# Optimization experiments

Measured on AMD Instinct MI355X. Metric: run time of the kernel, lower is better.

Reference implementation:

```python
import jax, jax.numpy as jnp
import numpy as np

SCENE_BOUND = 1.5

def _trilinear_sample(vol, g):
    """torch.nn.functional.grid_sample (3D, bilinear, zeros padding, align_corners=True).

    vol: (C, D, H, W) volume.
    g:   (N, 3) normalized coords in [-1, 1], ordered (x, y, z) where
         x indexes W, y indexes H, z indexes D (torch convention).
    returns: (N, C) interpolated features.
    """
    C, D, H, W = vol.shape
    sizes = jnp.array([W, H, D], dtype=g.dtype)
    pix = (g + 1.0) * 0.5 * (sizes - 1.0)  # align_corners=True mapping
    x, y, z = pix[:, 0], pix[:, 1], pix[:, 2]
    x0f, y0f, z0f = jnp.floor(x), jnp.floor(y), jnp.floor(z)
    fx, fy, fz = x - x0f, y - y0f, z - z0f
    x0, y0, z0 = x0f.astype(jnp.int32), y0f.astype(jnp.int32), z0f.astype(jnp.int32)
    vol_flat = vol.reshape(C, -1)  # (C, D*H*W)
    out = jnp.zeros((g.shape[0], C), dtype=vol.dtype)
    for dz in (0, 1):
        for dy in (0, 1):
            for dx in (0, 1):
                xi, yi, zi = x0 + dx, y0 + dy, z0 + dz
                w = ((fx if dx else 1.0 - fx)
                     * (fy if dy else 1.0 - fy)
                     * (fz if dz else 1.0 - fz))
                inb = ((xi >= 0) & (xi < W) & (yi >= 0) & (yi < H)
                       & (zi >= 0) & (zi < D))
                xi_c = jnp.clip(xi, 0, W - 1)
                yi_c = jnp.clip(yi, 0, H - 1)
                zi_c = jnp.clip(zi, 0, D - 1)
                flat = (zi_c * H + yi_c) * W + xi_c  # (N,)
                feat = jnp.take(vol_flat, flat, axis=1)  # (C, N)
                out = out + (w * inb.astype(w.dtype))[:, None] * feat.T
    return out


def setup_inputs() -> dict:
    key = jax.random.key(0)
    k1, k2, k3, k4, k5 = jax.random.split(key, 5)
    N, R = 2_000_000, 128
    xyz = (jax.random.uniform(k1, (N, 3), dtype=jnp.float32) * 2.0 - 1.0) * (SCENE_BOUND * 0.99)
    base_density = jax.random.normal(k2, (1, 1, R, R, R), dtype=jnp.float32)
    base_sh = jax.random.normal(k3, (1, 27, R, R, R), dtype=jnp.float32)
    detail_density = jax.random.normal(k4, (1, 1, R, R, R), dtype=jnp.float32) * 0.1
    detail_sh = jax.random.normal(k5, (1, 27, R, R, R), dtype=jnp.float32) * 0.1
    return {"xyz": xyz, "base_density": base_density, "base_sh": base_sh,
            "detail_density": detail_density, "detail_sh": detail_sh}


def reference(xyz, base_density, base_sh, detail_density, detail_sh):
    # grid property: concat(base_density + detail_density, base_sh + detail_sh)
    vol = jnp.concatenate([base_density + detail_density,
                           base_sh + detail_sh], axis=1)[0]  # (C, R, R, R)
    g = xyz / SCENE_BOUND  # normalized to [-1, 1]
    return _trilinear_sample(vol, g)  # (N, C), matches query()'s permuted output
```

## Files before the change

kernel.cpp:

```cpp
#include <hip/hip_runtime.h>
#include <hip/hip_fp16.h>
#include <cstdint>
#include <cstddef>

#define RR   128
#define VV   (RR * RR * RR)
#define NCH  28
#define CPAD 32

__device__ __forceinline__ unsigned short f2h(float f) {
    __half h = __float2half(f);
    return *reinterpret_cast<unsigned short*>(&h);
}
__device__ __forceinline__ float2 up2(unsigned int u) {
    __half2 h = *reinterpret_cast<__half2*>(&u);
    return __half22float2(h);
}

__global__ __launch_bounds__(256) void presum_kernel(
    const float* __restrict__ bden, const float* __restrict__ bsh,
    const float* __restrict__ dden, const float* __restrict__ dsh,
    unsigned short* __restrict__ ws)
{
    int tid = blockIdx.x * 256 + threadIdx.x;
    if (tid >= VV) return;

    unsigned short s[CPAD];
    s[0] = f2h(bden[tid] + dden[tid]);
#pragma unroll
    for (int c = 1; c < NCH; ++c) {
        size_t off = (size_t)(c - 1) * VV + tid;
        s[c] = f2h(bsh[off] + dsh[off]);
    }
#pragma unroll
    for (int c = NCH; c < CPAD; ++c) s[c] = 0;

    uint4* w = (uint4*)(ws + (size_t)tid * CPAD);
#pragma unroll
    for (int q = 0; q < 4; ++q) {
        uint4 v;
        v.x = (unsigned int)s[q*8+0] | ((unsigned int)s[q*8+1] << 16);
        v.y = (unsigned int)s[q*8+2] | ((unsigned int)s[q*8+3] << 16);
        v.z = (unsigned int)s[q*8+4] | ((unsigned int)s[q*8+5] << 16);
        v.w = (unsigned int)s[q*8+6] | ((unsigned int)s[q*8+7] << 16);
        w[q] = v;
    }
}

__global__ __launch_bounds__(256) void gather_kernel(
    const float* __restrict__ xyz,
    const unsigned short* __restrict__ vol,
    float* __restrict__ out, int N)
{
    int tid = blockIdx.x * 256 + threadIdx.x;
    int n = tid >> 2;
    int t = tid & 3;
    if (n >= N) return;

    const float* xp = xyz + (size_t)n * 3;
    const float S = 63.5f / 1.5f;
    float px = fmaf(xp[0], S, 63.5f);
    float py = fmaf(xp[1], S, 63.5f);
    float pz = fmaf(xp[2], S, 63.5f);
    float fx0 = floorf(px), fy0 = floorf(py), fz0 = floorf(pz);
    float fx = px - fx0, fy = py - fy0, fz = pz - fz0;
    int ix = (int)fx0, iy = (int)fy0, iz = (int)fz0;
    ix = min(max(ix, 0), RR - 2);
    iy = min(max(iy, 0), RR - 2);
    iz = min(max(iz, 0), RR - 2);

    float wx[2] = {1.0f - fx, fx};
    float wy[2] = {1.0f - fy, fy};
    float wz[2] = {1.0f - fz, fz};

    int ibase = (iz * RR + iy) * RR + ix;
    const char* basep = (const char*)vol + (size_t)t * 16;

    float acc[8];
#pragma unroll
    for (int k = 0; k < 8; ++k) acc[k] = 0.0f;

#pragma unroll
    for (int dz = 0; dz < 2; ++dz)
#pragma unroll
    for (int dy = 0; dy < 2; ++dy)
#pragma unroll
    for (int dx = 0; dx < 2; ++dx) {
        int vidx = ibase + dz * (RR * RR) + dy * RR + dx;
        float w = wz[dz] * wy[dy] * wx[dx];
        const uint4 q = *(const uint4*)(basep + (size_t)vidx * (CPAD * 2));
        float2 p0 = up2(q.x), p1 = up2(q.y), p2 = up2(q.z), p3 = up2(q.w);
        acc[0] = fmaf(w, p0.x, acc[0]);
        acc[1] = fmaf(w, p0.y, acc[1]);
        acc[2] = fmaf(w, p1.x, acc[2]);
        acc[3] = fmaf(w, p1.y, acc[3]);
        acc[4] = fmaf(w, p2.x, acc[4]);
        acc[5] = fmaf(w, p2.y, acc[5]);
        acc[6] = fmaf(w, p3.x, acc[6]);
        acc[7] = fmaf(w, p3.y, acc[7]);
    }

    float* op = out + (size_t)n * NCH + t * 8;
    if (t < 3) {
        *(float4*)op       = make_float4(acc[0], acc[1], acc[2], acc[3]);
        *(float4*)(op + 4) = make_float4(acc[4], acc[5], acc[6], acc[7]);
    } else {
        *(float4*)op = make_float4(acc[0], acc[1], acc[2], acc[3]);
    }
}

__global__ __launch_bounds__(256) void gather_fallback(
    const float* __restrict__ xyz,
    const float* __restrict__ bden, const float* __restrict__ bsh,
    const float* __restrict__ dden, const float* __restrict__ dsh,
    float* __restrict__ out, int N)
{
    int n = blockIdx.x * 256 + threadIdx.x;
    if (n >= N) return;
    const float* xp = xyz + (size_t)n * 3;
    const float S = 63.5f / 1.5f;
    float px = fmaf(xp[0], S, 63.5f);
    float py = fmaf(xp[1], S, 63.5f);
    float pz = fmaf(xp[2], S, 63.5f);
    float fx0 = floorf(px), fy0 = floorf(py), fz0 = floorf(pz);
    float fx = px - fx0, fy = py - fy0, fz = pz - fz0;
    int ix = (int)fx0, iy = (int)fy0, iz = (int)fz0;
    ix = min(max(ix, 0), RR - 2);
    iy = min(max(iy, 0), RR - 2);
    iz = min(max(iz, 0), RR - 2);
    float wx[2] = {1.0f - fx, fx}, wy[2] = {1.0f - fy, fy}, wz[2] = {1.0f - fz, fz};

    int idx[8]; float w[8];
#pragma unroll
    for (int k = 0; k < 8; ++k) {
        int dz = (k >> 2) & 1, dy = (k >> 1) & 1, dx = k & 1;
        idx[k] = ((iz + dz) * RR + (iy + dy)) * RR + (ix + dx);
        w[k] = wz[dz] * wy[dy] * wx[dx];
    }
#pragma unroll
    for (int c = 0; c < NCH; ++c) {
        const float* bp = (c == 0) ? bden : (bsh + (size_t)(c - 1) * VV);
        const float* dp = (c == 0) ? dden : (dsh + (size_t)(c - 1) * VV);
        float a = 0.0f;
#pragma unroll
        for (int k = 0; k < 8; ++k)
            a = fmaf(w[k], bp[idx[k]] + dp[idx[k]], a);
        out[(size_t)n * NCH + c] = a;
    }
}

extern "C" void kernel_launch(void* const* d_in, const int* in_sizes, int n_in,
                              void* d_out, int out_size, void* d_ws, size_t ws_size,
                              hipStream_t stream) {
    const float* xyz  = (const float*)d_in[0];
    const float* bden = (const float*)d_in[1];
    const float* bsh  = (const float*)d_in[2];
    const float* dden = (const float*)d_in[3];
    const float* dsh  = (const float*)d_in[4];
    float* out = (float*)d_out;
    int N = in_sizes[0] / 3;

    size_t need = (size_t)VV * CPAD * sizeof(unsigned short);
    if (ws_size >= need) {
        presum_kernel<<<(VV + 255) / 256, 256, 0, stream>>>(
            bden, bsh, dden, dsh, (unsigned short*)d_ws);
        long long threads = (long long)N * 4;
        gather_kernel<<<(unsigned int)((threads + 255) / 256), 256, 0, stream>>>(
            xyz, (const unsigned short*)d_ws, out, N);
    } else {
        gather_fallback<<<(N + 255) / 256, 256, 0, stream>>>(
            xyz, bden, bsh, dden, dsh, out, N);
    }
}
```

Baseline: 814.2 us.

## Bin points into 8^3 cells and gather from LDS-staged grid bricks

Replaces the full-volume fp16 presum plus global gather with a counting sort of points into 4096 spatial cells (histogram, scan, atomic scatter), followed by a per-cell kernel. That kernel loads a 9^3 brick of summed channels into shared memory as fp16 and interpolates every point in the cell from LDS. This removes the 117 MB packed-volume write and read and the random global gathers. In exchange it adds two passes over xyz, atomic contention on the cell counters, scattered output writes, and a 46 KB LDS tile per 512-thread block. The base-plus-detail sum is still computed every call, with halo columns read redundantly across neighbouring cells.

```diff
diff --git a/kernel.cpp b/kernel.cpp
--- a/kernel.cpp
+++ b/kernel.cpp
@@ -3,10 +3,15 @@
 #include <cstdint>
 #include <cstddef>
 
-#define RR   128
-#define VV   (RR * RR * RR)
-#define NCH  28
-#define CPAD 32
+#define RR     128
+#define VV     (RR * RR * RR)
+#define NCH    28
+#define CPAD   32
+#define CELL   8
+#define NCD    16
+#define NCELLS 4096
+#define REG    9
+#define RV     (REG * REG * REG)
 
 __device__ __forceinline__ unsigned short f2h(float f) {
     __half h = __float2half(f);
@@ -17,95 +22,163 @@
     return __half22float2(h);
 }
 
-__global__ __launch_bounds__(256) void presum_kernel(
+__device__ __forceinline__ void point_coords(float x, float y, float z,
+                                             float& px, float& py, float& pz,
+                                             int& ix, int& iy, int& iz) {
+    const float S = 63.5f / 1.5f;
+    px = fmaf(x, S, 63.5f);
+    py = fmaf(y, S, 63.5f);
+    pz = fmaf(z, S, 63.5f);
+    ix = min(max((int)floorf(px), 0), RR - 2);
+    iy = min(max((int)floorf(py), 0), RR - 2);
+    iz = min(max((int)floorf(pz), 0), RR - 2);
+}
+
+__global__ __launch_bounds__(256) void hist_kernel(
+    const float* __restrict__ xyz, unsigned int* __restrict__ cnt, int N)
+{
+    int n = blockIdx.x * 256 + threadIdx.x;
+    if (n >= N) return;
+    const float* xp = xyz + (size_t)n * 3;
+    float px, py, pz; int ix, iy, iz;
+    point_coords(xp[0], xp[1], xp[2], px, py, pz, ix, iy, iz);
+    int cell = ((iz >> 3) * NCD + (iy >> 3)) * NCD + (ix >> 3);
+    atomicAdd(&cnt[cell], 1u);
+}
+
+__global__ __launch_bounds__(256) void scan_kernel(
+    const unsigned int* __restrict__ cnt,
+    unsigned int* __restrict__ off,
+    unsigned int* __restrict__ cur)
+{
+    __shared__ unsigned int part[256];
+    int t = threadIdx.x;
+    unsigned int local[16];
+    unsigned int s = 0;
+#pragma unroll
+    for (int i = 0; i < 16; ++i) { local[i] = cnt[t * 16 + i]; s += local[i]; }
+    part[t] = s;
+    __syncthreads();
+    for (int d = 1; d < 256; d <<= 1) {
+        unsigned int v = (t >= d) ? part[t - d] : 0u;
+        __syncthreads();
+        part[t] += v;
+        __syncthreads();
+    }
+    unsigned int base = (t == 0) ? 0u : part[t - 1];
+#pragma unroll
+    for (int i = 0; i < 16; ++i) {
+        off[t * 16 + i] = base;
+        cur[t * 16 + i] = base;
+        base += local[i];
+    }
+    if (t == 255) off[NCELLS] = part[255];
+}
+
+__global__ __launch_bounds__(256) void scatter_kernel(
+    const float* __restrict__ xyz, unsigned int* __restrict__ cur,
+    float4* __restrict__ sorted, int N)
+{
+    int n = blockIdx.x * 256 + threadIdx.x;
+    if (n >= N) return;
+    const float* xp = xyz + (size_t)n * 3;
+    float px, py, pz; int ix, iy, iz;
+    point_coords(xp[0], xp[1], xp[2], px, py, pz, ix, iy, iz);
+    int cell = ((iz >> 3) * NCD + (iy >> 3)) * NCD + (ix >> 3);
+    unsigned int slot = atomicAdd(&cur[cell], 1u);
+    sorted[slot] = make_float4(px, py, pz, __int_as_float(n));
+}
+
+__global__ __launch_bounds__(512) void cell_gather(
     const float* __restrict__ bden, const float* __restrict__ bsh,
     const float* __restrict__ dden, const float* __restrict__ dsh,
-    unsigned short* __restrict__ ws)
-{
-    int tid = blockIdx.x * 256 + threadIdx.x;
-    if (tid >= VV) return;
-
-    unsigned short s[CPAD];
-    s[0] = f2h(bden[tid] + dden[tid]);
-#pragma unroll
-    for (int c = 1; c < NCH; ++c) {
-        size_t off = (size_t)(c - 1) * VV + tid;
-        s[c] = f2h(bsh[off] + dsh[off]);
-    }
-#pragma unroll
-    for (int c = NCH; c < CPAD; ++c) s[c] = 0;
-
-    uint4* w = (uint4*)(ws + (size_t)tid * CPAD);
-#pragma unroll
-    for (int q = 0; q < 4; ++q) {
-        uint4 v;
-        v.x = (unsigned int)s[q*8+0] | ((unsigned int)s[q*8+1] << 16);
-        v.y = (unsigned int)s[q*8+2] | ((unsigned int)s[q*8+3] << 16);
-        v.z = (unsigned int)s[q*8+4] | ((unsigned int)s[q*8+5] << 16);
-        v.w = (unsigned int)s[q*8+6] | ((unsigned int)s[q*8+7] << 16);
-        w[q] = v;
-    }
-}
-
-__global__ __launch_bounds__(256) void gather_kernel(
-    const float* __restrict__ xyz,
-    const unsigned short* __restrict__ vol,
-    float* __restrict__ out, int N)
-{
-    int tid = blockIdx.x * 256 + threadIdx.x;
-    int n = tid >> 2;
-    int t = tid & 3;
-    if (n >= N) return;
-
-    const float* xp = xyz + (size_t)n * 3;
-    const float S = 63.5f / 1.5f;
-    float px = fmaf(xp[0], S, 63.5f);
-    float py = fmaf(xp[1], S, 63.5f);
-    float pz = fmaf(xp[2], S, 63.5f);
-    float fx0 = floorf(px), fy0 = floorf(py), fz0 = floorf(pz);
-    float fx = px - fx0, fy = py - fy0, fz = pz - fz0;
-    int ix = (int)fx0, iy = (int)fy0, iz = (int)fz0;
-    ix = min(max(ix, 0), RR - 2);
-    iy = min(max(iy, 0), RR - 2);
-    iz = min(max(iz, 0), RR - 2);
-
-    float wx[2] = {1.0f - fx, fx};
-    float wy[2] = {1.0f - fy, fy};
-    float wz[2] = {1.0f - fz, fz};
-
-    int ibase = (iz * RR + iy) * RR + ix;
-    const char* basep = (const char*)vol + (size_t)t * 16;
-
-    float acc[8];
-#pragma unroll
-    for (int k = 0; k < 8; ++k) acc[k] = 0.0f;
-
-#pragma unroll
-    for (int dz = 0; dz < 2; ++dz)
-#pragma unroll
-    for (int dy = 0; dy < 2; ++dy)
-#pragma unroll
-    for (int dx = 0; dx < 2; ++dx) {
-        int vidx = ibase + dz * (RR * RR) + dy * RR + dx;
-        float w = wz[dz] * wy[dy] * wx[dx];
-        const uint4 q = *(const uint4*)(basep + (size_t)vidx * (CPAD * 2));
-        float2 p0 = up2(q.x), p1 = up2(q.y), p2 = up2(q.z), p3 = up2(q.w);
-        acc[0] = fmaf(w, p0.x, acc[0]);
-        acc[1] = fmaf(w, p0.y, acc[1]);
-        acc[2] = fmaf(w, p1.x, acc[2]);
-        acc[3] = fmaf(w, p1.y, acc[3]);
-        acc[4] = fmaf(w, p2.x, acc[4]);
-        acc[5] = fmaf(w, p2.y, acc[5]);
-        acc[6] = fmaf(w, p3.x, acc[6]);
-        acc[7] = fmaf(w, p3.y, acc[7]);
-    }
-
-    float* op = out + (size_t)n * NCH + t * 8;
-    if (t < 3) {
-        *(float4*)op       = make_float4(acc[0], acc[1], acc[2], acc[3]);
-        *(float4*)(op + 4) = make_float4(acc[4], acc[5], acc[6], acc[7]);
-    } else {
-        *(float4*)op = make_float4(acc[0], acc[1], acc[2], acc[3]);
+    const float4* __restrict__ sorted, const unsigned int* __restrict__ off,
+    float* __restrict__ out)
+{
+    __shared__ unsigned short vlds[RV * CPAD];
+
+    int bid = blockIdx.x;
+    int cid = (bid & 7) * (NCELLS / 8) + (bid >> 3);
+    int cx = cid & 15, cy = (cid >> 4) & 15, cz = cid >> 8;
+    int x0 = cx << 3, y0 = cy << 3, z0 = cz << 3;
+    int xlast = (cx == 15) ? 7 : 8;
+
+    for (int task = threadIdx.x; task < 81 * CPAD; task += 512) {
+        int c = task / 81;
+        int r = task - c * 81;
+        int rz = r / 9, ry = r - rz * 9;
+        int v0 = (rz * 9 + ry) * 9;
+        if (c < NCH) {
+            int zg = min(z0 + rz, RR - 1);
+            int yg = min(y0 + ry, RR - 1);
+            size_t row = ((size_t)(zg * RR + yg)) * RR + x0;
+            const float* bp; const float* dp;
+            if (c == 0) { bp = bden + row; dp = dden + row; }
+            else { size_t o = (size_t)(c - 1) * VV + row; bp = bsh + o; dp = dsh + o; }
+            float s[9];
+#pragma unroll
+            for (int xx = 0; xx < 8; ++xx) s[xx] = bp[xx] + dp[xx];
+            s[8] = bp[xlast] + dp[xlast];
+#pragma unroll
+            for (int xx = 0; xx < 9; ++xx)
+                vlds[(v0 + xx) * CPAD + c] = f2h(s[xx]);
+        } else {
+#pragma unroll
+            for (int xx = 0; xx < 9; ++xx)
+                vlds[(v0 + xx) * CPAD + c] = 0;
+        }
+    }
+    __syncthreads();
+
+    int start = (int)off[cid], end = (int)off[cid + 1];
+    int g = threadIdx.x >> 2, t = threadIdx.x & 3;
+
+    for (int p = start + g; p < end; p += 128) {
+        float4 pt = sorted[p];
+        float px = pt.x, py = pt.y, pz = pt.z;
+        int idx = __float_as_int(pt.w);
+
+        float fx0 = floorf(px), fy0 = floorf(py), fz0 = floorf(pz);
+        float fx = px - fx0, fy = py - fy0, fz = pz - fz0;
+        int lx = min(max((int)fx0, 0), RR - 2) - x0;
+        int ly = min(max((int)fy0, 0), RR - 2) - y0;
+        int lz = min(max((int)fz0, 0), RR - 2) - z0;
+
+        float wx[2] = {1.0f - fx, fx};
+        float wy[2] = {1.0f - fy, fy};
+        float wz[2] = {1.0f - fz, fz};
+
+        float acc[8];
+#pragma unroll
+        for (int k = 0; k < 8; ++k) acc[k] = 0.0f;
+
+#pragma unroll
+        for (int dz = 0; dz < 2; ++dz)
+#pragma unroll
+        for (int dy = 0; dy < 2; ++dy)
+#pragma unroll
+        for (int dx = 0; dx < 2; ++dx) {
+            int v = ((lz + dz) * 9 + (ly + dy)) * 9 + (lx + dx);
+            float w = wz[dz] * wy[dy] * wx[dx];
+            const uint4 q = *(const uint4*)(vlds + v * CPAD + t * 8);
+            float2 p0 = up2(q.x), p1 = up2(q.y), p2 = up2(q.z), p3 = up2(q.w);
+            acc[0] = fmaf(w, p0.x, acc[0]);
+            acc[1] = fmaf(w, p0.y, acc[1]);
+            acc[2] = fmaf(w, p1.x, acc[2]);
+            acc[3] = fmaf(w, p1.y, acc[3]);
+            acc[4] = fmaf(w, p2.x, acc[4]);
+            acc[5] = fmaf(w, p2.y, acc[5]);
+            acc[6] = fmaf(w, p3.x, acc[6]);
+            acc[7] = fmaf(w, p3.y, acc[7]);
+        }
+
+        float* op = out + (size_t)idx * NCH + t * 8;
+        if (t < 3) {
+            *(float4*)op       = make_float4(acc[0], acc[1], acc[2], acc[3]);
+            *(float4*)(op + 4) = make_float4(acc[4], acc[5], acc[6], acc[7]);
+        } else {
+            *(float4*)op = make_float4(acc[0], acc[1], acc[2], acc[3]);
+        }
     }
 }
 
@@ -118,16 +191,9 @@
     int n = blockIdx.x * 256 + threadIdx.x;
     if (n >= N) return;
     const float* xp = xyz + (size_t)n * 3;
-    const float S = 63.5f / 1.5f;
-    float px = fmaf(xp[0], S, 63.5f);
-    float py = fmaf(xp[1], S, 63.5f);
-    float pz = fmaf(xp[2], S, 63.5f);
-    float fx0 = floorf(px), fy0 = floorf(py), fz0 = floorf(pz);
-    float fx = px - fx0, fy = py - fy0, fz = pz - fz0;
-    int ix = (int)fx0, iy = (int)fy0, iz = (int)fz0;
-    ix = min(max(ix, 0), RR - 2);
-    iy = min(max(iy, 0), RR - 2);
-    iz = min(max(iz, 0), RR - 2);
+    float px, py, pz; int ix, iy, iz;
+    point_coords(xp[0], xp[1], xp[2], px, py, pz, ix, iy, iz);
+    float fx = px - floorf(px), fy = py - floorf(py), fz = pz - floorf(pz);
     float wx[2] = {1.0f - fx, fx}, wy[2] = {1.0f - fy, fy}, wz[2] = {1.0f - fz, fz};
 
     int idx[8]; float w[8];
@@ -160,13 +226,21 @@
     float* out = (float*)d_out;
     int N = in_sizes[0] / 3;
 
-    size_t need = (size_t)VV * CPAD * sizeof(unsigned short);
+    size_t sortBytes = (size_t)N * sizeof(float4);
+    size_t need = sortBytes + (size_t)(NCELLS + (NCELLS + 1) + NCELLS) * 4;
+
     if (ws_size >= need) {
-        presum_kernel<<<(VV + 255) / 256, 256, 0, stream>>>(
-            bden, bsh, dden, dsh, (unsigned short*)d_ws);
-        long long threads = (long long)N * 4;
-        gather_kernel<<<(unsigned int)((threads + 255) / 256), 256, 0, stream>>>(
-            xyz, (const unsigned short*)d_ws, out, N);
+        char* w = (char*)d_ws;
+        float4* sorted    = (float4*)w;
+        unsigned int* cnt = (unsigned int*)(w + sortBytes);
+        unsigned int* off = cnt + NCELLS;
+        unsigned int* cur = off + NCELLS + 1;
+
+        hipMemsetAsync(cnt, 0, NCELLS * sizeof(unsigned int), stream);
+        hist_kernel<<<(N + 255) / 256, 256, 0, stream>>>(xyz, cnt, N);
+        scan_kernel<<<1, 256, 0, stream>>>(cnt, off, cur);
+        scatter_kernel<<<(N + 255) / 256, 256, 0, stream>>>(xyz, cur, sorted, N);
+        cell_gather<<<NCELLS, 512, 0, stream>>>(bden, bsh, dden, dsh, sorted, off, out);
     } else {
         gather_fallback<<<(N + 255) / 256, 256, 0, stream>>>(
             xyz, bden, bsh, dden, dsh, out, N);
```

After: 1.046 ms. 28.5% more time.
